# Kernel optimization log

Hardware: AMD Instinct MI355X
Metric: run time of the kernel (lower is better)

Reference implementation:

```python
import jax, jax.numpy as jnp
import numpy as np

N_USERS = 100000
N_ITEMS = 50000
N_NODES = N_USERS + N_ITEMS
NNZ = 3200000
DIM = 64
N_LAYERS = 3
BATCH = 8192


def setup_inputs() -> dict:
    key = jax.random.key(0)
    ks = jax.random.split(key, 8)
    user_emb = jax.random.normal(ks[0], (N_USERS, DIM), dtype=jnp.float32) * 0.1
    item_emb0 = jnp.zeros((N_ITEMS, DIM), dtype=jnp.float32)
    edge_val = jax.random.uniform(ks[1], (NNZ,), dtype=jnp.float32)
    W = jax.random.normal(ks[2], (DIM, DIM), dtype=jnp.float32) / np.sqrt(DIM)
    b = jax.random.normal(ks[3], (DIM,), dtype=jnp.float32) * 0.01
    edge_src = jax.random.randint(ks[4], (NNZ,), 0, N_NODES, dtype=jnp.int32)
    edge_dst = jax.random.randint(ks[5], (NNZ,), 0, N_NODES, dtype=jnp.int32)
    users = jax.random.randint(ks[6], (BATCH,), 0, N_USERS, dtype=jnp.int32)
    items = jax.random.randint(ks[7], (BATCH,), 0, N_ITEMS, dtype=jnp.int32)
    return {"user_emb": user_emb, "item_emb0": item_emb0, "edge_val": edge_val,
            "W": W, "b": b, "edge_src": edge_src, "edge_dst": edge_dst,
            "users": users, "items": items}


def _spmm(edge_src, edge_dst, edge_val, x):
    # y[dst] += val * x[src]  -- COO SpMM via segment_sum
    msgs = edge_val[:, None] * x[edge_src]          # [nnz, d]
    return jax.ops.segment_sum(msgs, edge_dst, num_segments=N_NODES)


def reference(user_emb, item_emb0, edge_val, W, b, edge_src, edge_dst, users, items):
    all_emb = jnp.concatenate([user_emb, item_emb0], axis=0)  # [N, d]
    embs = [all_emb]
    for _ in range(N_LAYERS):
        all_emb = _spmm(edge_src, edge_dst, edge_val, all_emb)
        embs.append(all_emb)
    # per-layer: transform item slice, keep ORIGINAL user_emb for user slice
    new_embs = []
    for e in embs:
        item_t = e[N_USERS:] @ W.T + b                 # Linear(d, d)
        new_embs.append(jnp.concatenate([user_emb, item_t], axis=0))
    light_out = jnp.mean(jnp.stack(new_embs, axis=1), axis=1)  # [N, d]
    all_users = light_out[:N_USERS]
    all_items = light_out[N_USERS:]
    users_emb = all_users[users]
    items_emb = all_items[items]
    gamma = jnp.sum(users_emb * items_emb, axis=1)     # [B]
    return gamma
```

## Files before the change

### kernel.cpp

```cpp
#include <hip/hip_runtime.h>
#include <hip/hip_fp16.h>

#define N_USERS 100000
#define N_ITEMS 50000
#define N_NODES 150000
#define NNZ     3200000
#define DIM     64
#define BATCH   8192

#define BKT_SHIFT 10
#define BKTSZ     (1 << BKT_SHIFT)
#define NBKT      ((N_NODES + BKTSZ - 1) >> BKT_SHIFT)
#define SRC_MASK  0x3FFFF

#define P1_THREADS 512
#define P1_PER_T   16
#define P1_CHUNK   (P1_THREADS * P1_PER_T)
#define P1_BLOCKS  ((NNZ + P1_CHUNK - 1) / P1_CHUNK)

#define SLOTS_ALL  150016

#define NB_HIST 512
#define NB_CONV 768
#define NB_MARK 32
#define NB_BUILD1 (NB_HIST + NB_CONV + NB_MARK)


__global__ __launch_bounds__(256) void k_zero_i32(int* __restrict__ p, int n) {
    for (int i = blockIdx.x * blockDim.x + threadIdx.x; i < n; i += gridDim.x * blockDim.x)
        p[i] = 0;
}

__global__ __launch_bounds__(256) void k_build1(const int* __restrict__ dst,
                                                const float4* __restrict__ ue,
                                                const int* __restrict__ items,
                                                int* __restrict__ gh,
                                                uint2* __restrict__ xu,
                                                int* __restrict__ used) {
    __shared__ int h[NBKT];
    const int b = blockIdx.x, t = threadIdx.x;
    if (b < NB_HIST) {
        for (int i = t; i < NBKT; i += 256) h[i] = 0;
        __syncthreads();
        for (int i = b * 256 + t; i < NNZ; i += NB_HIST * 256)
            atomicAdd(&h[dst[i] >> BKT_SHIFT], 1);
        __syncthreads();
        for (int i = t; i < NBKT; i += 256) atomicAdd(&gh[i], h[i]);
    } else if (b < NB_HIST + NB_CONV) {
        const int n = N_USERS * 16;
        for (int i = (b - NB_HIST) * 256 + t; i < n; i += NB_CONV * 256) {
            float4 v = ue[i];
            union { unsigned u; __half2 hh; } a0, a1;
            a0.hh = __floats2half2_rn(v.x, v.y);
            a1.hh = __floats2half2_rn(v.z, v.w);
            xu[i] = make_uint2(a0.u, a1.u);
        }
    } else {
        const int i = (b - NB_HIST - NB_CONV) * 256 + t;
        if (i < BATCH) used[items[i]] = 1;
    }
}

__global__ __launch_bounds__(256) void k_scan147(const int* __restrict__ gh,
                                                 int* __restrict__ bbase,
                                                 int* __restrict__ bhead,
                                                 int* __restrict__ rp) {
    __shared__ int sh[256];
    const int t = threadIdx.x;
    int v = (t < NBKT) ? gh[t] : 0;
    sh[t] = v; __syncthreads();
    for (int o = 1; o < 256; o <<= 1) {
        int a = (t >= o) ? sh[t - o] : 0;
        __syncthreads();
        sh[t] += a;
        __syncthreads();
    }
    int ex = sh[t] - v;
    if (t < NBKT) { bbase[t] = ex; bhead[t] = ex; }
    if (t == 0)   { bbase[NBKT] = NNZ; rp[N_NODES] = NNZ; }
}

__global__ __launch_bounds__(P1_THREADS) void k_pass1(const int* __restrict__ src,
                                                      const int* __restrict__ dst,
                                                      const float* __restrict__ val,
                                                      int* __restrict__ bhead,
                                                      unsigned* __restrict__ tmp1,
                                                      unsigned short* __restrict__ tmp2) {
    __shared__ int cnt[NBKT];
    __shared__ int base[NBKT];
    const int t = threadIdx.x;
    const int c0 = blockIdx.x * P1_CHUNK;
    for (int i = t; i < NBKT; i += P1_THREADS) cnt[i] = 0;
    __syncthreads();
    unsigned pk[P1_PER_T]; unsigned short qv[P1_PER_T];
    int rk[P1_PER_T], bk[P1_PER_T];
    #pragma unroll
    for (int k = 0; k < P1_PER_T; ++k) {
        const int i = c0 + k * P1_THREADS + t;
        if (i < NNZ) {
            const int d = dst[i];
            bk[k] = d >> BKT_SHIFT;
            pk[k] = (unsigned)src[i] | ((unsigned)(d & (BKTSZ - 1)) << 18);
            qv[k] = (unsigned short)(val[i] * 16383.f + 0.5f);
            rk[k] = atomicAdd(&cnt[bk[k]], 1);
        } else bk[k] = -1;
    }
    __syncthreads();
    for (int i = t; i < NBKT; i += P1_THREADS) base[i] = atomicAdd(&bhead[i], cnt[i]);
    __syncthreads();
    #pragma unroll
    for (int k = 0; k < P1_PER_T; ++k)
        if (bk[k] >= 0) {
            const int pos = base[bk[k]] + rk[k];
            tmp1[pos] = pk[k];
            tmp2[pos] = qv[k];
        }
}

__global__ __launch_bounds__(1024) void k_bucket(const int* __restrict__ bbase,
                                                 const unsigned* __restrict__ tmp1,
                                                 const unsigned short* __restrict__ tmp2,
                                                 unsigned* __restrict__ edges,
                                                 int* __restrict__ rp,
                                                 int* __restrict__ ucnt) {
    __shared__ int cnt[BKTSZ * 2];
    __shared__ int wtot[16];
    const int b = blockIdx.x, t = threadIdx.x;
    const int start = bbase[b], end = bbase[b + 1];
    cnt[t] = 0; cnt[t + BKTSZ] = 0;
    __syncthreads();
    for (int i = start + t; i < end; i += 1024) {
        const unsigned x = tmp1[i];
        const int dloc = (x >> 18) & (BKTSZ - 1);
        const int cls = ((x & SRC_MASK) >= N_USERS) ? 1 : 0;
        atomicAdd(&cnt[dloc * 2 + cls], 1);
    }
    __syncthreads();
    const int c0 = cnt[2 * t], c1 = cnt[2 * t + 1];
    const int s = c0 + c1;
    const int lane = t & 63;
    const int w = t >> 6;
    int inc = s;
    #pragma unroll
    for (int o = 1; o < 64; o <<= 1) {
        const int v = __shfl_up(inc, o);
        if (lane >= o) inc += v;
    }
    if (lane == 63) wtot[w] = inc;
    __syncthreads();
    if (t == 0) {
        int run = 0;
        #pragma unroll
        for (int i = 0; i < 16; ++i) { const int x = wtot[i]; wtot[i] = run; run += x; }
    }
    __syncthreads();
    const int ex = wtot[w] + inc - s;
    const int node = (b << BKT_SHIFT) + t;
    if (node < N_NODES) { rp[node] = start + ex; ucnt[node] = c0; }
    cnt[2 * t] = ex;
    cnt[2 * t + 1] = ex + c0;
    __syncthreads();
    for (int i = start + t; i < end; i += 1024) {
        const unsigned x = tmp1[i];
        const unsigned q = tmp2[i];
        const int src  = (int)(x & SRC_MASK);
        const int dloc = (x >> 18) & (BKTSZ - 1);
        const int cls  = (src >= N_USERS) ? 1 : 0;
        const int pos = atomicAdd(&cnt[dloc * 2 + cls], 1);
        edges[start + pos] = (x & SRC_MASK) | (q << 18);
    }
}

__global__ __launch_bounds__(256) void k_spmm0(const int* __restrict__ rp,
                                               const int* __restrict__ ucnt,
                                               const unsigned* __restrict__ edges,
                                               const uint2* __restrict__ x16,
                                               uint2* __restrict__ y16,
                                               float4* __restrict__ isum4,
                                               const int* __restrict__ used) {
    __shared__ int s_nin[32], s_deg[32], s_node[32];
    const int t = threadIdx.x;
    if (t < 32) {
        const int slot = blockIdx.x * 32 + t;
        int node = (slot < N_NODES) ? slot : -1;
        int deg = (node >= 0) ? ucnt[node] : 0;
        s_nin[t] = node; s_deg[t] = deg;
    }
    __syncthreads();
    if (t < 32) {
        const int d = s_deg[t];
        int r = 0;
        #pragma unroll
        for (int j = 0; j < 32; ++j) {
            const int dj = s_deg[j];
            r += (dj > d) || (dj == d && j < t);
        }
        s_node[r] = s_nin[t];
    }
    __syncthreads();

    const int lane = t & 63;
    const int g16 = ((t >> 6) << 2) + (lane >> 4);
    const int q = lane & 15;
    const int nA = s_node[2 * g16];
    const int nB = s_node[2 * g16 + 1];

    int begA = 0, degA = 0, begB = 0, degB = 0;
    if (nA >= 0) { begA = rp[nA]; degA = ucnt[nA]; }
    if (nB >= 0) { begB = rp[nB]; degB = ucnt[nB]; }

    const int  l8  = lane & 7;
    const bool isB = (lane & 8) != 0;
    const int  mybeg = isB ? begB : begA;
    const int  mydeg = isB ? degB : degA;
    const int  gbase = lane & 48;

    float4 accA = make_float4(0.f, 0.f, 0.f, 0.f);
    float4 accB = make_float4(0.f, 0.f, 0.f, 0.f);
    const int itA = (degA + 7) >> 3, itB = (degB + 7) >> 3;
    const int nit = (itA > itB) ? itA : itB;

    for (int it = 0; it < nit; ++it) {
        const int bb = it << 3;
        const int dmy = bb + l8;
        const unsigned my_e = (dmy < mydeg) ? edges[mybeg + dmy] : 0u;
        int sA[8], sB[8]; float vA[8], vB[8];
        #pragma unroll
        for (int k = 0; k < 8; ++k) {
            const unsigned eA = __shfl(my_e, gbase + k);
            const unsigned eB = __shfl(my_e, gbase + 8 + k);
            sA[k] = (int)(eA & SRC_MASK);
            vA[k] = (float)(eA >> 18) * (1.0f / 16383.0f);
            sB[k] = (int)(eB & SRC_MASK);
            vB[k] = (float)(eB >> 18) * (1.0f / 16383.0f);
        }
        uint2 rA[8], rB[8];
        #pragma unroll
        for (int k = 0; k < 8; ++k) rA[k] = x16[(size_t)sA[k] * 16 + q];
        #pragma unroll
        for (int k = 0; k < 8; ++k) rB[k] = x16[(size_t)sB[k] * 16 + q];
        #pragma unroll
        for (int k = 0; k < 8; ++k) {
            union { unsigned u; __half2 h; } c0, c1;
            c0.u = rA[k].x; c1.u = rA[k].y;
            const float2 f0 = __half22float2(c0.h);
            const float2 f1 = __half22float2(c1.h);
            accA.x = fmaf(vA[k], f0.x, accA.x);
            accA.y = fmaf(vA[k], f0.y, accA.y);
            accA.z = fmaf(vA[k], f1.x, accA.z);
            accA.w = fmaf(vA[k], f1.y, accA.w);
        }
        #pragma unroll
        for (int k = 0; k < 8; ++k) {
            union { unsigned u; __half2 h; } c0, c1;
            c0.u = rB[k].x; c1.u = rB[k].y;
            const float2 f0 = __half22float2(c0.h);
            const float2 f1 = __half22float2(c1.h);
            accB.x = fmaf(vB[k], f0.x, accB.x);
            accB.y = fmaf(vB[k], f0.y, accB.y);
            accB.z = fmaf(vB[k], f1.x, accB.z);
            accB.w = fmaf(vB[k], f1.y, accB.w);
        }
    }

    #pragma unroll
    for (int half = 0; half < 2; ++half) {
        const int node = half ? nB : nA;
        const float4 acc = half ? accB : accA;
        if (node < 0) continue;
        union { unsigned u; __half2 h; } a0, a1;
        a0.h = __floats2half2_rn(acc.x, acc.y);
        a1.h = __floats2half2_rn(acc.z, acc.w);
        y16[(size_t)node * 16 + q] = make_uint2(a0.u, a1.u);
        if (node >= N_USERS) {
            const int in = node - N_USERS;
            if (used[in] == 1) isum4[(size_t)in * 16 + q] = acc;
        }
    }
}

__global__ __launch_bounds__(256) void k_spmm1(const int* __restrict__ rp,
                                               const unsigned* __restrict__ edges,
                                               const uint2* __restrict__ x16,
                                               uint2* __restrict__ y16,
                                               float4* __restrict__ isum4,
                                               const int* __restrict__ used) {
    __shared__ int s_nin[16], s_deg[16], s_node[16];
    const int t = threadIdx.x;
    if (t < 16) {
        const int node = blockIdx.x * 16 + t;
        s_nin[t] = node;
        s_deg[t] = rp[node + 1] - rp[node];
    }
    __syncthreads();
    if (t < 16) {
        const int d = s_deg[t];
        int r = 0;
        #pragma unroll
        for (int j = 0; j < 16; ++j) {
            const int dj = s_deg[j];
            r += (dj > d) || (dj == d && j < t);
        }
        s_node[r] = s_nin[t];
    }
    __syncthreads();

    const int lane = t & 63;
    const int g = lane >> 4, q = lane & 15;
    const int node = s_node[((t >> 6) << 2) + g];
    const int beg = rp[node];
    const int deg = rp[node + 1] - beg;
    const int l8 = lane & 7;
    const int gbase = lane & 48;

    float4 acc = make_float4(0.f, 0.f, 0.f, 0.f);
    for (int bb = 0; bb < deg; bb += 8) {
        const int dmy = bb + l8;
        const unsigned my_e = (dmy < deg) ? edges[beg + dmy] : 0u;
        int se[8]; float ve[8];
        #pragma unroll
        for (int k = 0; k < 8; ++k) {
            const unsigned e = __shfl(my_e, gbase + k);
            se[k] = (int)(e & SRC_MASK);
            ve[k] = (float)(e >> 18) * (1.0f / 16383.0f);
        }
        uint2 rw[8];
        #pragma unroll
        for (int k = 0; k < 8; ++k)
            rw[k] = x16[(size_t)se[k] * 16 + q];
        #pragma unroll
        for (int k = 0; k < 8; ++k) {
            union { unsigned u; __half2 h; } c0, c1;
            c0.u = rw[k].x; c1.u = rw[k].y;
            const float2 f0 = __half22float2(c0.h);
            const float2 f1 = __half22float2(c1.h);
            acc.x = fmaf(ve[k], f0.x, acc.x);
            acc.y = fmaf(ve[k], f0.y, acc.y);
            acc.z = fmaf(ve[k], f1.x, acc.z);
            acc.w = fmaf(ve[k], f1.y, acc.w);
        }
    }

    union { unsigned u; __half2 h; } a0, a1;
    a0.h = __floats2half2_rn(acc.x, acc.y);
    a1.h = __floats2half2_rn(acc.z, acc.w);
    y16[(size_t)node * 16 + q] = make_uint2(a0.u, a1.u);
    if (node >= N_USERS) {
        const int in = node - N_USERS;
        if (used[in] == 1) {
            const size_t io = (size_t)in * 16 + q;
            float4 tv = isum4[io];
            tv.x += acc.x; tv.y += acc.y; tv.z += acc.z; tv.w += acc.w;
            isum4[io] = tv;
        }
    }
}

__global__ __launch_bounds__(256) void k_final(const float* __restrict__ ue,
                                               const float* __restrict__ isum,
                                               const float* __restrict__ W,
                                               const float* __restrict__ bvec,
                                               const int* __restrict__ users,
                                               const int* __restrict__ items,
                                               const int* __restrict__ rp,
                                               const unsigned* __restrict__ edges,
                                               const __half* __restrict__ xh,
                                               float* __restrict__ out) {
    __shared__ float Ws[DIM * DIM];
    const int t = threadIdx.x;
    for (int i = t; i < DIM * DIM; i += 256) Ws[i] = W[i];
    __syncthreads();

    const int gw = blockIdx.x * 4 + (t >> 6);
    const int lane = t & 63;
    if (gw >= BATCH) return;
    const int u  = users[gw];
    const int it = items[gw];

    const float u_l = ue[(size_t)u * DIM + lane];

    const int node = N_USERS + it;
    const int beg = rp[node];
    const int deg = rp[node + 1] - beg;
    float macc = 0.0f;
    for (int bb = 0; bb < deg; bb += 4) {
        int ss[4]; float vv[4];
        #pragma unroll
        for (int k = 0; k < 4; ++k) {
            const bool ok = (bb + k) < deg;
            const unsigned e = edges[ok ? (beg + bb + k) : beg];
            ss[k] = ok ? (int)(e & SRC_MASK) : 0;
            vv[k] = ok ? (float)(e >> 18) * (1.0f / 16383.0f) : 0.f;
        }
        __half hv[4];
        #pragma unroll
        for (int k = 0; k < 4; ++k)
            hv[k] = xh[(size_t)ss[k] * DIM + lane];
        #pragma unroll
        for (int k = 0; k < 4; ++k)
            macc = fmaf(vv[k], __half2float(hv[k]), macc);
    }

    const float m_l = (isum[(size_t)it * DIM + lane] + macc) * 0.25f;
    const float b_l = bvec[lane];

    float v = 0.0f;
    for (int j = 0; j < DIM; ++j) {
        float uj = __shfl(u_l, j);
        v = fmaf(uj, Ws[j * DIM + lane], v);
    }
    float p = fmaf(v, m_l, u_l * b_l);
    for (int o = 32; o > 0; o >>= 1) p += __shfl_xor(p, o);
    if (lane == 0) out[gw] = p;
}

extern "C" void kernel_launch(void* const* d_in, const int* in_sizes, int n_in,
                              void* d_out, int out_size, void* d_ws, size_t ws_size,
                              hipStream_t stream) {
    const float* user_emb  = (const float*)d_in[0];
    const float* item_emb0 = (const float*)d_in[1];
    const float* edge_val  = (const float*)d_in[2];
    const float* W         = (const float*)d_in[3];
    const float* bvec      = (const float*)d_in[4];
    const int*   edge_src  = (const int*)d_in[5];
    const int*   edge_dst  = (const int*)d_in[6];
    const int*   users     = (const int*)d_in[7];
    const int*   items     = (const int*)d_in[8];
    float* out = (float*)d_out;
    (void)item_emb0;

    char* ws = (char*)d_ws;
    uint2*          bufA16  = (uint2*)         (ws + 0);
    uint2*          bufB16  = (uint2*)         (ws + 19200000);
    uint2*          xu16    = (uint2*)         (ws + 38400000);
    float*          itemsum = (float*)         (ws + 51200000);
    unsigned*       edges   = (unsigned*)      (ws + 64000000);
    unsigned*       tmp1    = (unsigned*)      (ws + 76800000);
    unsigned short* tmp2    = (unsigned short*)(ws + 89600000);
    int*            rp      = (int*)           (ws + 96000000);
    int*            ucnt    = (int*)           (ws + 96600064);
    int*            ghist   = (int*)           (ws + 97200064);
    int*            bbase   = (int*)           (ws + 97201088);
    int*            bhead   = (int*)           (ws + 97202112);
    int*            used    = (int*)           (ws + 97203136);

    k_zero_i32<<<256, 256, 0, stream>>>(ghist, 50768);

    k_build1<<<NB_BUILD1, 256, 0, stream>>>(edge_dst, (const float4*)user_emb,
                                            items, ghist, xu16, used);

    k_scan147<<<1, 256, 0, stream>>>(ghist, bbase, bhead, rp);

    k_pass1<<<P1_BLOCKS, P1_THREADS, 0, stream>>>(edge_src, edge_dst, edge_val,
                                                  bhead, tmp1, tmp2);
    k_bucket<<<NBKT, 1024, 0, stream>>>(bbase, tmp1, tmp2, edges, rp, ucnt);

    k_spmm0<<<SLOTS_ALL / 32, 256, 0, stream>>>(rp, ucnt, edges, xu16,
                                                bufB16, (float4*)itemsum, used);
    k_spmm1<<<N_NODES / 16, 256, 0, stream>>>(rp, edges, bufB16,
                                              bufA16, (float4*)itemsum, used);

    k_final<<<BATCH / 4, 256, 0, stream>>>(user_emb, itemsum, W, bvec,
                                           users, items, rp, edges,
                                           (const __half*)bufA16, out);
}
```

Before: 215.1 us.

## Replace histogram+scan with fixed-capacity padded buckets and fuse build kernels

```diff
diff --git a/kernel.cpp b/kernel.cpp
--- a/kernel.cpp
+++ b/kernel.cpp
@@ -8,47 +8,72 @@
 #define DIM     64
 #define BATCH   8192
 
-#define BKT_SHIFT 10
+#define BKT_SHIFT 9
 #define BKTSZ     (1 << BKT_SHIFT)
 #define NBKT      ((N_NODES + BKTSZ - 1) >> BKT_SHIFT)
+#define BPAD      12288
 #define SRC_MASK  0x3FFFF
 
 #define P1_THREADS 512
 #define P1_PER_T   16
 #define P1_CHUNK   (P1_THREADS * P1_PER_T)
-#define P1_BLOCKS  ((NNZ + P1_CHUNK - 1) / P1_CHUNK)
+#define NB_P1      ((NNZ + P1_CHUNK - 1) / P1_CHUNK)
 
 #define SLOTS_ALL  150016
 
-#define NB_HIST 512
-#define NB_CONV 768
-#define NB_MARK 32
-#define NB_BUILD1 (NB_HIST + NB_CONV + NB_MARK)
-
-
-__global__ __launch_bounds__(256) void k_zero_i32(int* __restrict__ p, int n) {
-    for (int i = blockIdx.x * blockDim.x + threadIdx.x; i < n; i += gridDim.x * blockDim.x)
-        p[i] = 0;
-}
-
-__global__ __launch_bounds__(256) void k_build1(const int* __restrict__ dst,
-                                                const float4* __restrict__ ue,
-                                                const int* __restrict__ items,
-                                                int* __restrict__ gh,
-                                                uint2* __restrict__ xu,
-                                                int* __restrict__ used) {
-    __shared__ int h[NBKT];
+#define NB_CONV 384
+#define NB_MARK 16
+#define NB_BUILD (NB_P1 + NB_CONV + NB_MARK)
+
+
+__global__ __launch_bounds__(512) void k_zero_small(int* __restrict__ p, int n) {
+    const int i = threadIdx.x;
+    if (i < n) p[i] = 0;
+}
+
+__global__ __launch_bounds__(512) void k_build(const int* __restrict__ src,
+                                               const int* __restrict__ dst,
+                                               const float* __restrict__ val,
+                                               const float4* __restrict__ ue,
+                                               const int* __restrict__ items,
+                                               int* __restrict__ bhead,
+                                               unsigned* __restrict__ tmp1,
+                                               unsigned short* __restrict__ tmp2,
+                                               uint2* __restrict__ xu,
+                                               int* __restrict__ used) {
     const int b = blockIdx.x, t = threadIdx.x;
-    if (b < NB_HIST) {
-        for (int i = t; i < NBKT; i += 256) h[i] = 0;
+    if (b < NB_P1) {
+        __shared__ int cnt[NBKT];
+        __shared__ int base[NBKT];
+        const int c0 = b * P1_CHUNK;
+        for (int i = t; i < NBKT; i += P1_THREADS) cnt[i] = 0;
         __syncthreads();
-        for (int i = b * 256 + t; i < NNZ; i += NB_HIST * 256)
-            atomicAdd(&h[dst[i] >> BKT_SHIFT], 1);
+        unsigned pk[P1_PER_T]; unsigned short qv[P1_PER_T];
+        int rk[P1_PER_T], bk[P1_PER_T];
+        #pragma unroll
+        for (int k = 0; k < P1_PER_T; ++k) {
+            const int i = c0 + k * P1_THREADS + t;
+            if (i < NNZ) {
+                const int d = dst[i];
+                bk[k] = d >> BKT_SHIFT;
+                pk[k] = (unsigned)src[i] | ((unsigned)(d & (BKTSZ - 1)) << 18);
+                qv[k] = (unsigned short)(val[i] * 16383.f + 0.5f);
+                rk[k] = atomicAdd(&cnt[bk[k]], 1);
+            } else bk[k] = -1;
+        }
         __syncthreads();
-        for (int i = t; i < NBKT; i += 256) atomicAdd(&gh[i], h[i]);
-    } else if (b < NB_HIST + NB_CONV) {
+        for (int i = t; i < NBKT; i += P1_THREADS) base[i] = atomicAdd(&bhead[i], cnt[i]);
+        __syncthreads();
+        #pragma unroll
+        for (int k = 0; k < P1_PER_T; ++k)
+            if (bk[k] >= 0) {
+                const int pos = bk[k] * BPAD + base[bk[k]] + rk[k];
+                tmp1[pos] = pk[k];
+                tmp2[pos] = qv[k];
+            }
+    } else if (b < NB_P1 + NB_CONV) {
         const int n = N_USERS * 16;
-        for (int i = (b - NB_HIST) * 256 + t; i < n; i += NB_CONV * 256) {
+        for (int i = (b - NB_P1) * 512 + t; i < n; i += NB_CONV * 512) {
             float4 v = ue[i];
             union { unsigned u; __half2 hh; } a0, a1;
             a0.hh = __floats2half2_rn(v.x, v.y);
@@ -56,81 +81,26 @@
             xu[i] = make_uint2(a0.u, a1.u);
         }
     } else {
-        const int i = (b - NB_HIST - NB_CONV) * 256 + t;
-        if (i < BATCH) used[items[i]] = 1;
-    }
-}
-
-__global__ __launch_bounds__(256) void k_scan147(const int* __restrict__ gh,
-                                                 int* __restrict__ bbase,
-                                                 int* __restrict__ bhead,
-                                                 int* __restrict__ rp) {
-    __shared__ int sh[256];
-    const int t = threadIdx.x;
-    int v = (t < NBKT) ? gh[t] : 0;
-    sh[t] = v; __syncthreads();
-    for (int o = 1; o < 256; o <<= 1) {
-        int a = (t >= o) ? sh[t - o] : 0;
-        __syncthreads();
-        sh[t] += a;
-        __syncthreads();
-    }
-    int ex = sh[t] - v;
-    if (t < NBKT) { bbase[t] = ex; bhead[t] = ex; }
-    if (t == 0)   { bbase[NBKT] = NNZ; rp[N_NODES] = NNZ; }
-}
-
-__global__ __launch_bounds__(P1_THREADS) void k_pass1(const int* __restrict__ src,
-                                                      const int* __restrict__ dst,
-                                                      const float* __restrict__ val,
-                                                      int* __restrict__ bhead,
-                                                      unsigned* __restrict__ tmp1,
-                                                      unsigned short* __restrict__ tmp2) {
-    __shared__ int cnt[NBKT];
-    __shared__ int base[NBKT];
-    const int t = threadIdx.x;
-    const int c0 = blockIdx.x * P1_CHUNK;
-    for (int i = t; i < NBKT; i += P1_THREADS) cnt[i] = 0;
-    __syncthreads();
-    unsigned pk[P1_PER_T]; unsigned short qv[P1_PER_T];
-    int rk[P1_PER_T], bk[P1_PER_T];
-    #pragma unroll
-    for (int k = 0; k < P1_PER_T; ++k) {
-        const int i = c0 + k * P1_THREADS + t;
-        if (i < NNZ) {
-            const int d = dst[i];
-            bk[k] = d >> BKT_SHIFT;
-            pk[k] = (unsigned)src[i] | ((unsigned)(d & (BKTSZ - 1)) << 18);
-            qv[k] = (unsigned short)(val[i] * 16383.f + 0.5f);
-            rk[k] = atomicAdd(&cnt[bk[k]], 1);
-        } else bk[k] = -1;
-    }
-    __syncthreads();
-    for (int i = t; i < NBKT; i += P1_THREADS) base[i] = atomicAdd(&bhead[i], cnt[i]);
-    __syncthreads();
-    #pragma unroll
-    for (int k = 0; k < P1_PER_T; ++k)
-        if (bk[k] >= 0) {
-            const int pos = base[bk[k]] + rk[k];
-            tmp1[pos] = pk[k];
-            tmp2[pos] = qv[k];
-        }
-}
-
-__global__ __launch_bounds__(1024) void k_bucket(const int* __restrict__ bbase,
-                                                 const unsigned* __restrict__ tmp1,
-                                                 const unsigned short* __restrict__ tmp2,
-                                                 unsigned* __restrict__ edges,
-                                                 int* __restrict__ rp,
-                                                 int* __restrict__ ucnt) {
+        const int i = (b - NB_P1 - NB_CONV) * 512 + t;
+        used[items[i]] = 1;
+    }
+}
+
+__global__ __launch_bounds__(512) void k_bucket(const int* __restrict__ bhead,
+                                                const unsigned* __restrict__ tmp1,
+                                                const unsigned short* __restrict__ tmp2,
+                                                unsigned* __restrict__ edges,
+                                                int* __restrict__ rp,
+                                                int* __restrict__ dcu) {
     __shared__ int cnt[BKTSZ * 2];
-    __shared__ int wtot[16];
+    __shared__ int wtot[8];
     const int b = blockIdx.x, t = threadIdx.x;
-    const int start = bbase[b], end = bbase[b + 1];
+    const int start = b * BPAD;
+    const int nedge = bhead[b];
     cnt[t] = 0; cnt[t + BKTSZ] = 0;
     __syncthreads();
-    for (int i = start + t; i < end; i += 1024) {
-        const unsigned x = tmp1[i];
+    for (int i = t; i < nedge; i += 512) {
+        const unsigned x = tmp1[start + i];
         const int dloc = (x >> 18) & (BKTSZ - 1);
         const int cls = ((x & SRC_MASK) >= N_USERS) ? 1 : 0;
         atomicAdd(&cnt[dloc * 2 + cls], 1);
@@ -151,28 +121,30 @@
     if (t == 0) {
         int run = 0;
         #pragma unroll
-        for (int i = 0; i < 16; ++i) { const int x = wtot[i]; wtot[i] = run; run += x; }
+        for (int i = 0; i < 8; ++i) { const int x = wtot[i]; wtot[i] = run; run += x; }
     }
     __syncthreads();
     const int ex = wtot[w] + inc - s;
     const int node = (b << BKT_SHIFT) + t;
-    if (node < N_NODES) { rp[node] = start + ex; ucnt[node] = c0; }
+    if (node < N_NODES) {
+        rp[node]  = start + ex;
+        dcu[node] = (s << 16) | c0;
+    }
     cnt[2 * t] = ex;
     cnt[2 * t + 1] = ex + c0;
     __syncthreads();
-    for (int i = start + t; i < end; i += 1024) {
-        const unsigned x = tmp1[i];
-        const unsigned q = tmp2[i];
-        const int src  = (int)(x & SRC_MASK);
+    for (int i = t; i < nedge; i += 512) {
+        const unsigned x = tmp1[start + i];
+        const unsigned q = tmp2[start + i];
         const int dloc = (x >> 18) & (BKTSZ - 1);
-        const int cls  = (src >= N_USERS) ? 1 : 0;
+        const int cls  = ((x & SRC_MASK) >= N_USERS) ? 1 : 0;
         const int pos = atomicAdd(&cnt[dloc * 2 + cls], 1);
         edges[start + pos] = (x & SRC_MASK) | (q << 18);
     }
 }
 
 __global__ __launch_bounds__(256) void k_spmm0(const int* __restrict__ rp,
-                                               const int* __restrict__ ucnt,
+                                               const int* __restrict__ dcu,
                                                const unsigned* __restrict__ edges,
                                                const uint2* __restrict__ x16,
                                                uint2* __restrict__ y16,
@@ -183,7 +155,7 @@
     if (t < 32) {
         const int slot = blockIdx.x * 32 + t;
         int node = (slot < N_NODES) ? slot : -1;
-        int deg = (node >= 0) ? ucnt[node] : 0;
+        int deg = (node >= 0) ? (dcu[node] & 0xFFFF) : 0;
         s_nin[t] = node; s_deg[t] = deg;
     }
     __syncthreads();
@@ -206,8 +178,8 @@
     const int nB = s_node[2 * g16 + 1];
 
     int begA = 0, degA = 0, begB = 0, degB = 0;
-    if (nA >= 0) { begA = rp[nA]; degA = ucnt[nA]; }
-    if (nB >= 0) { begB = rp[nB]; degB = ucnt[nB]; }
+    if (nA >= 0) { begA = rp[nA]; degA = dcu[nA] & 0xFFFF; }
+    if (nB >= 0) { begB = rp[nB]; degB = dcu[nB] & 0xFFFF; }
 
     const int  l8  = lane & 7;
     const bool isB = (lane & 8) != 0;
@@ -280,6 +252,7 @@
 }
 
 __global__ __launch_bounds__(256) void k_spmm1(const int* __restrict__ rp,
+                                               const int* __restrict__ dcu,
                                                const unsigned* __restrict__ edges,
                                                const uint2* __restrict__ x16,
                                                uint2* __restrict__ y16,
@@ -290,7 +263,7 @@
     if (t < 16) {
         const int node = blockIdx.x * 16 + t;
         s_nin[t] = node;
-        s_deg[t] = rp[node + 1] - rp[node];
+        s_deg[t] = dcu[node] >> 16;
     }
     __syncthreads();
     if (t < 16) {
@@ -309,7 +282,7 @@
     const int g = lane >> 4, q = lane & 15;
     const int node = s_node[((t >> 6) << 2) + g];
     const int beg = rp[node];
-    const int deg = rp[node + 1] - beg;
+    const int deg = dcu[node] >> 16;
     const int l8 = lane & 7;
     const int gbase = lane & 48;
 
@@ -363,6 +336,7 @@
                                                const int* __restrict__ users,
                                                const int* __restrict__ items,
                                                const int* __restrict__ rp,
+                                               const int* __restrict__ dcu,
                                                const unsigned* __restrict__ edges,
                                                const __half* __restrict__ xh,
                                                float* __restrict__ out) {
@@ -381,7 +355,7 @@
 
     const int node = N_USERS + it;
     const int beg = rp[node];
-    const int deg = rp[node + 1] - beg;
+    const int deg = dcu[node] >> 16;
     float macc = 0.0f;
     for (int bb = 0; bb < deg; bb += 4) {
         int ss[4]; float vv[4];
@@ -435,32 +409,27 @@
     uint2*          xu16    = (uint2*)         (ws + 38400000);
     float*          itemsum = (float*)         (ws + 51200000);
     unsigned*       edges   = (unsigned*)      (ws + 64000000);
-    unsigned*       tmp1    = (unsigned*)      (ws + 76800000);
-    unsigned short* tmp2    = (unsigned short*)(ws + 89600000);
-    int*            rp      = (int*)           (ws + 96000000);
-    int*            ucnt    = (int*)           (ws + 96600064);
-    int*            ghist   = (int*)           (ws + 97200064);
-    int*            bbase   = (int*)           (ws + 97201088);
-    int*            bhead   = (int*)           (ws + 97202112);
-    int*            used    = (int*)           (ws + 97203136);
-
-    k_zero_i32<<<256, 256, 0, stream>>>(ghist, 50768);
-
-    k_build1<<<NB_BUILD1, 256, 0, stream>>>(edge_dst, (const float4*)user_emb,
-                                            items, ghist, xu16, used);
-
-    k_scan147<<<1, 256, 0, stream>>>(ghist, bbase, bhead, rp);
-
-    k_pass1<<<P1_BLOCKS, P1_THREADS, 0, stream>>>(edge_src, edge_dst, edge_val,
-                                                  bhead, tmp1, tmp2);
-    k_bucket<<<NBKT, 1024, 0, stream>>>(bbase, tmp1, tmp2, edges, rp, ucnt);
-
-    k_spmm0<<<SLOTS_ALL / 32, 256, 0, stream>>>(rp, ucnt, edges, xu16,
+    unsigned*       tmp1    = (unsigned*)      (ws + 78401536);
+    unsigned short* tmp2    = (unsigned short*)(ws + 92803072);
+    int*            rp      = (int*)           (ws + 100003840);
+    int*            dcu     = (int*)           (ws + 100603840);
+    int*            bhead   = (int*)           (ws + 101203840);
+    int*            used    = (int*)           (ws + 101205056);
+
+    k_zero_small<<<1, 512, 0, stream>>>(bhead, NBKT);
+
+    k_build<<<NB_BUILD, 512, 0, stream>>>(edge_src, edge_dst, edge_val,
+                                          (const float4*)user_emb, items,
+                                          bhead, tmp1, tmp2, xu16, used);
+
+    k_bucket<<<NBKT, 512, 0, stream>>>(bhead, tmp1, tmp2, edges, rp, dcu);
+
+    k_spmm0<<<SLOTS_ALL / 32, 256, 0, stream>>>(rp, dcu, edges, xu16,
                                                 bufB16, (float4*)itemsum, used);
-    k_spmm1<<<N_NODES / 16, 256, 0, stream>>>(rp, edges, bufB16,
+    k_spmm1<<<N_NODES / 16, 256, 0, stream>>>(rp, dcu, edges, bufB16,
                                               bufA16, (float4*)itemsum, used);
 
     k_final<<<BATCH / 4, 256, 0, stream>>>(user_emb, itemsum, W, bvec,
-                                           users, items, rp, edges,
+                                           users, items, rp, dcu, edges,
                                            (const __half*)bufA16, out);
 }
```

Result: faster. 198.7 us (-7.6%).
